# Optimization experiments

Measured on AMD Instinct MI355X. Metric: run time of the kernel, lower is better.

## Reference

```python
import jax, jax.numpy as jnp
import numpy as np

NUM_HEADS = 16
NUM_HIDDENS = 1024
NEG_INF = -1e6


def setup_inputs() -> dict:
    key = jax.random.key(0)
    ks = jax.random.split(key, 8)
    B, S, D = 2, 2048, NUM_HIDDENS
    scale = 1.0 / np.sqrt(D)
    return {
        "q": jax.random.normal(ks[0], (B, S, D), jnp.float32),
        "k": jax.random.normal(ks[1], (B, S, D), jnp.float32),
        "v": jax.random.normal(ks[2], (B, S, D), jnp.float32),
        # nn.Linear weights have shape (out_features, in_features)
        "Wq": jax.random.normal(ks[3], (D, D), jnp.float32) * scale,
        "Wk": jax.random.normal(ks[4], (D, D), jnp.float32) * scale,
        "Wv": jax.random.normal(ks[5], (D, D), jnp.float32) * scale,
        "Wo": jax.random.normal(ks[6], (D, D), jnp.float32) * scale,
        "valid_len": jax.random.randint(ks[7], (B,), 1, 2048 + 1, jnp.int32),
    }


def _unpack_heads(x, nh):
    # (B, S, H) -> (B*nh, S, H//nh), matching Unpack_base_head
    B, S, H = x.shape
    return x.reshape(B, S, nh, H // nh).transpose(0, 2, 1, 3).reshape(B * nh, S, H // nh)


def _merge_heads(x, nh):
    # Faithful to Merge_base_head: (B*nh, S, dh) -> (B, nh, S, dh)
    # -> permute(0,2,3,1) -> (B, S, dh, nh) -> (B, S, dh*nh)
    Bnh, S, dh = x.shape
    B = Bnh // nh
    x = x.reshape(B, nh, S, dh).transpose(0, 2, 3, 1)
    return x.reshape(B, S, dh * nh)


def reference(q, k, v, Wq, Wk, Wv, Wo, valid_len):
    nh = NUM_HEADS
    # projections (bias=False); Linear: x @ W.T
    qh = _unpack_heads(q @ Wq.T, nh)  # (B*nh, S, dh)
    kh = _unpack_heads(k @ Wk.T, nh)
    vh = _unpack_heads(v @ Wv.T, nh)
    dh = qh.shape[-1]
    scores = jnp.einsum("bqd,bkd->bqk", qh, kh) / jnp.sqrt(jnp.float32(dh))
    # repeat_interleave valid_len by num_heads along dim 0
    vl = jnp.repeat(valid_len, nh)  # (B*nh,)
    key_pos = jnp.arange(scores.shape[-1])  # (S,)
    mask = key_pos[None, None, :] < vl[:, None, None]  # (B*nh, 1, S)
    scores = jnp.where(mask, scores, NEG_INF)
    attn = jax.nn.softmax(scores, axis=-1)  # dropout=0.0 (eval) -> identity
    out = jnp.einsum("bqk,bkd->bqd", attn, vh)  # (B*nh, S, dh)
    out = _merge_heads(out, nh) @ Wo.T  # (B, S, H)
    return out, attn
```

## Files before the change

kernel.cpp:

```cpp
#include <hip/hip_runtime.h>
#include <stdint.h>

#define SB 2048
#define DB 1024
#define NHB 16
#define DHB 64

typedef __attribute__((ext_vector_type(8))) short short8;
typedef __attribute__((ext_vector_type(4))) short short4v;
typedef __attribute__((ext_vector_type(4))) float f32x4;

#define SC2 0.18033688011112042f

__device__ __forceinline__ unsigned short f2bf(float f) {
  union { float f; uint32_t u; } v; v.f = f;
  uint32_t u = v.u;
  return (unsigned short)((u + 0x7FFFu + ((u >> 16) & 1u)) >> 16);
}

__device__ __forceinline__ void gld16(const void* g, void* l) {
  __builtin_amdgcn_global_load_lds(
      (const __attribute__((address_space(1))) void*)g,
      (__attribute__((address_space(3))) void*)l, 16, 0, 0);
}

__device__ __forceinline__ int xcd_swz(int bid, int nwg) {
  return (bid & 7) * (nwg >> 3) + (bid >> 3);
}

struct ConvArgs {
  const float* s[6];
  unsigned short* d[6];
  int n[6];
};

__global__ __launch_bounds__(256) void conv_kernel(ConvArgs a,
                                                   const float* __restrict__ Wo,
                                                   unsigned short* __restrict__ Wob) {
  const int t = blockIdx.y;
  if (t == 6) {
    for (int i = blockIdx.x * 256 + threadIdx.x; i < DB * DB; i += gridDim.x * 256) {
      int o = i >> 10, cp = i & 1023;
      int src = (o << 10) + ((cp & 63) << 4) + (cp >> 6);
      Wob[i] = f2bf(Wo[src]);
    }
    return;
  }
  const float* __restrict__ src = a.s[t];
  unsigned short* __restrict__ dst = a.d[t];
  const int n8 = a.n[t] >> 3;
  for (int i = blockIdx.x * 256 + threadIdx.x; i < n8; i += gridDim.x * 256) {
    const f32x4* p = (const f32x4*)src + (size_t)i * 2;
    f32x4 x = p[0], y = p[1];
    short8 o;
    o[0] = (short)f2bf(x[0]); o[1] = (short)f2bf(x[1]);
    o[2] = (short)f2bf(x[2]); o[3] = (short)f2bf(x[3]);
    o[4] = (short)f2bf(y[0]); o[5] = (short)f2bf(y[1]);
    o[6] = (short)f2bf(y[2]); o[7] = (short)f2bf(y[3]);
    *(short8*)(dst + (size_t)i * 8) = o;
  }
}

struct GemmArgs {
  const unsigned short* A[3];
  const unsigned short* B[3];
  void* O[3];
  int mode[3];
};

__global__ __launch_bounds__(256) void gemm128(GemmArgs ga) {
  __shared__ unsigned short SH[17408];
  unsigned short* Ab = SH;
  unsigned short* Bb = SH + 8192;

  const int z = blockIdx.y;
  const unsigned short* __restrict__ A = ga.A[z];
  const unsigned short* __restrict__ Bw = ga.B[z];
  const int mode = ga.mode[z];

  const int tid = threadIdx.x;
  const int w = tid >> 6, lane = tid & 63;
  const int g = lane >> 4, li = lane & 15;
  const int wm = w >> 1, wn = w & 1;
  const int l = xcd_swz(blockIdx.x, 256);
  const int m0 = (l >> 3) * 128, n0 = (l & 7) * 128;

  const int srow = lane >> 3;
  const int sg = (lane & 7) ^ srow;

  f32x4 acc[4][4];
  #pragma unroll
  for (int i = 0; i < 4; ++i)
    #pragma unroll
    for (int j = 0; j < 4; ++j)
      #pragma unroll
      for (int e = 0; e < 4; ++e) acc[i][j][e] = 0.f;

  for (int k0 = 0; k0 < DB; k0 += 64) {
    __syncthreads();
    #pragma unroll
    for (int i = 0; i < 4; ++i) {
      int c = w * 4 + i;
      gld16(A + (size_t)(m0 + c * 8 + srow) * DB + k0 + sg * 8, Ab + c * 512);
      gld16(Bw + (size_t)(n0 + c * 8 + srow) * DB + k0 + sg * 8, Bb + c * 512);
    }
    __syncthreads();
    short8 af[4][2], bf[4][2];
    #pragma unroll
    for (int mf = 0; mf < 4; ++mf)
      #pragma unroll
      for (int ks = 0; ks < 2; ++ks)
        af[mf][ks] = *(const short8*)&Ab[(wm * 64 + mf * 16 + li) * 64 +
                                         (((ks * 4 + g) ^ (li & 7)) << 3)];
    #pragma unroll
    for (int nf = 0; nf < 4; ++nf)
      #pragma unroll
      for (int ks = 0; ks < 2; ++ks)
        bf[nf][ks] = *(const short8*)&Bb[(wn * 64 + nf * 16 + li) * 64 +
                                         (((ks * 4 + g) ^ (li & 7)) << 3)];
    __builtin_amdgcn_s_setprio(1);
    #pragma unroll
    for (int ks = 0; ks < 2; ++ks)
      #pragma unroll
      for (int mf = 0; mf < 4; ++mf)
        #pragma unroll
        for (int nf = 0; nf < 4; ++nf)
          acc[mf][nf] = __builtin_amdgcn_mfma_f32_16x16x32_bf16(
              af[mf][ks], bf[nf][ks], acc[mf][nf], 0, 0, 0);
    __builtin_amdgcn_s_setprio(0);
  }

  if (mode == 0) {
    unsigned short* O = (unsigned short*)ga.O[z];
    #pragma unroll
    for (int mf = 0; mf < 4; ++mf)
      #pragma unroll
      for (int nf = 0; nf < 4; ++nf)
        #pragma unroll
        for (int r = 0; r < 4; ++r) {
          int row = m0 + wm * 64 + mf * 16 + g * 4 + r;
          int col = n0 + wn * 64 + nf * 16 + li;
          int b_ = row >> 11, s_ = row & 2047;
          int h = col >> 6, dp = col & 63;
          O[((size_t)(b_ * NHB + h) * SB + s_) * DHB + dp] = f2bf(acc[mf][nf][r]);
        }
  } else {
    unsigned short* O = (unsigned short*)ga.O[z];
    __syncthreads();
    #pragma unroll
    for (int mf = 0; mf < 4; ++mf)
      #pragma unroll
      for (int nf = 0; nf < 4; ++nf) {
        short4v pk;
        #pragma unroll
        for (int r = 0; r < 4; ++r) pk[r] = (short)f2bf(acc[mf][nf][r]);
        *(short4v*)&SH[(size_t)(wn * 64 + nf * 16 + li) * 136 +
                       wm * 64 + mf * 16 + g * 4] = pk;
      }
    __syncthreads();
    int c = tid >> 1, rh = tid & 1;
    int col = n0 + c;
    int h = col >> 6, dp = col & 63;
    int b_ = m0 >> 11, s0 = (m0 & 2047) + rh * 64;
    unsigned short* dst = O + ((size_t)(b_ * NHB + h) * DHB + dp) * SB + s0;
    #pragma unroll
    for (int j = 0; j < 8; ++j)
      *(short8*)(dst + j * 8) = *(const short8*)&SH[c * 136 + rh * 64 + j * 8];
  }
}

__global__ __launch_bounds__(256) void attn_kernel(
    const unsigned short* __restrict__ Qh, const unsigned short* __restrict__ Kh,
    const unsigned short* __restrict__ Vt, const int* __restrict__ valid_len,
    float* __restrict__ attn_out, unsigned short* __restrict__ Mg)
{
  __shared__ unsigned short Kb[2][4096];
  __shared__ unsigned short Vb[2][4096];
  __shared__ unsigned short P[128][72];

  const int tid = threadIdx.x;
  const int wave = tid >> 6, lane = tid & 63;
  const int g = lane >> 4, li = lane & 15;
  const int lsw = xcd_swz(blockIdx.x, 512);
  const int xcd = lsw >> 6, j = lsw & 63;
  const int bh = ((j >> 5) << 4) + xcd * 2 + ((j >> 4) & 1);
  const int q0 = (j & 15) * 128;
  const int b_ = bh >> 4;
  const int vl = valid_len[b_];
  const int nkt = min(32, (vl + 63) >> 6);

  const int srow = lane >> 3;
  const int sg = (lane & 7) ^ srow;

  const size_t kbase = (size_t)bh * SB * DHB;
  const size_t vbase = (size_t)bh * DHB * SB;

  short8 qa[2][2];
  #pragma unroll
  for (int qf = 0; qf < 2; ++qf)
    #pragma unroll
    for (int ks = 0; ks < 2; ++ks)
      qa[qf][ks] = *(const short8*)(
          Qh + ((size_t)bh * SB + q0 + wave * 32 + qf * 16 + li) * DHB +
          ks * 32 + g * 8);

  float lQ[2] = {0.f, 0.f};

  {
    const int c = wave * 2;
    gld16(Kh + kbase + (size_t)(c * 8 + srow) * DHB + sg * 8, &Kb[0][c * 512]);
    gld16(Kh + kbase + (size_t)((c + 1) * 8 + srow) * DHB + sg * 8,
          &Kb[0][(c + 1) * 512]);
    int cur = 0;
    for (int kti = 0; kti < nkt; ++kti) {
      __syncthreads();
      if (kti + 1 < nkt) {
        int kn = (kti + 1) * 64;
        gld16(Kh + kbase + (size_t)(kn + c * 8 + srow) * DHB + sg * 8,
              &Kb[cur ^ 1][c * 512]);
        gld16(Kh + kbase + (size_t)(kn + (c + 1) * 8 + srow) * DHB + sg * 8,
              &Kb[cur ^ 1][(c + 1) * 512]);
      }
      const int kt = kti * 64;
      f32x4 sc[2][4];
      #pragma unroll
      for (int qf = 0; qf < 2; ++qf)
        #pragma unroll
        for (int nf = 0; nf < 4; ++nf)
          #pragma unroll
          for (int e = 0; e < 4; ++e) sc[qf][nf][e] = 0.f;
      __builtin_amdgcn_s_setprio(1);
      #pragma unroll
      for (int ks = 0; ks < 2; ++ks)
        #pragma unroll
        for (int nf = 0; nf < 4; ++nf) {
          short8 kbf = *(const short8*)&Kb[cur][(nf * 16 + li) * 64 +
                                               (((ks * 4 + g) ^ (li & 7)) << 3)];
          #pragma unroll
          for (int qf = 0; qf < 2; ++qf)
            sc[qf][nf] = __builtin_amdgcn_mfma_f32_16x16x32_bf16(
                kbf, qa[qf][ks], sc[qf][nf], 0, 0, 0);
        }
      __builtin_amdgcn_s_setprio(0);
      if (kt + 64 <= vl) {
        #pragma unroll
        for (int qf = 0; qf < 2; ++qf) {
          float la = 0.f;
          #pragma unroll
          for (int nf = 0; nf < 4; ++nf)
            #pragma unroll
            for (int r = 0; r < 4; ++r) la += exp2f(sc[qf][nf][r] * SC2);
          lQ[qf] += la;
        }
      } else {
        #pragma unroll
        for (int qf = 0; qf < 2; ++qf) {
          float la = 0.f;
          #pragma unroll
          for (int nf = 0; nf < 4; ++nf)
            #pragma unroll
            for (int r = 0; r < 4; ++r) {
              int key = kt + nf * 16 + g * 4 + r;
              float s2 = (key < vl) ? sc[qf][nf][r] * SC2 : -1.5e6f;
              la += exp2f(s2);
            }
          lQ[qf] += la;
        }
      }
      cur ^= 1;
    }
  }
  __syncthreads();

  float rlQ[2];
  #pragma unroll
  for (int qf = 0; qf < 2; ++qf) {
    float L = lQ[qf];
    L += __shfl_xor(L, 16);
    L += __shfl_xor(L, 32);
    rlQ[qf] = 1.f / L;
  }

  f32x4 oacc[2][4];
  #pragma unroll
  for (int qf = 0; qf < 2; ++qf)
    #pragma unroll
    for (int nf = 0; nf < 4; ++nf)
      #pragma unroll
      for (int e = 0; e < 4; ++e) oacc[qf][nf][e] = 0.f;

  {
    const int c = wave * 2;
    gld16(Kh + kbase + (size_t)(c * 8 + srow) * DHB + sg * 8, &Kb[0][c * 512]);
    gld16(Kh + kbase + (size_t)((c + 1) * 8 + srow) * DHB + sg * 8,
          &Kb[0][(c + 1) * 512]);
    gld16(Vt + vbase + (size_t)(c * 8 + srow) * SB + sg * 8, &Vb[0][c * 512]);
    gld16(Vt + vbase + (size_t)((c + 1) * 8 + srow) * SB + sg * 8,
          &Vb[0][(c + 1) * 512]);
    asm volatile("s_waitcnt vmcnt(0)\n\ts_barrier" ::: "memory");
    int cur = 0;
    for (int kti = 0; kti < nkt; ++kti) {
      if (kti + 1 < nkt) {
        int kn = (kti + 1) * 64;
        gld16(Kh + kbase + (size_t)(kn + c * 8 + srow) * DHB + sg * 8,
              &Kb[cur ^ 1][c * 512]);
        gld16(Kh + kbase + (size_t)(kn + (c + 1) * 8 + srow) * DHB + sg * 8,
              &Kb[cur ^ 1][(c + 1) * 512]);
        gld16(Vt + vbase + (size_t)(c * 8 + srow) * SB + kn + sg * 8,
              &Vb[cur ^ 1][c * 512]);
        gld16(Vt + vbase + (size_t)((c + 1) * 8 + srow) * SB + kn + sg * 8,
              &Vb[cur ^ 1][(c + 1) * 512]);
      }
      const int kt = kti * 64;
      f32x4 sc[2][4];
      #pragma unroll
      for (int qf = 0; qf < 2; ++qf)
        #pragma unroll
        for (int nf = 0; nf < 4; ++nf)
          #pragma unroll
          for (int e = 0; e < 4; ++e) sc[qf][nf][e] = 0.f;
      __builtin_amdgcn_s_setprio(1);
      #pragma unroll
      for (int ks = 0; ks < 2; ++ks)
        #pragma unroll
        for (int nf = 0; nf < 4; ++nf) {
          short8 kbf = *(const short8*)&Kb[cur][(nf * 16 + li) * 64 +
                                               (((ks * 4 + g) ^ (li & 7)) << 3)];
          #pragma unroll
          for (int qf = 0; qf < 2; ++qf)
            sc[qf][nf] = __builtin_amdgcn_mfma_f32_16x16x32_bf16(
                kbf, qa[qf][ks], sc[qf][nf], 0, 0, 0);
        }
      __builtin_amdgcn_s_setprio(0);
      const bool fullt = (kt + 64 <= vl);
      #pragma unroll
      for (int qf = 0; qf < 2; ++qf) {
        const int qrow = q0 + wave * 32 + qf * 16 + li;
        #pragma unroll
        for (int nf = 0; nf < 4; ++nf) {
          short4v pk;
          if (fullt) {
            #pragma unroll
            for (int r = 0; r < 4; ++r) {
              float p = exp2f(sc[qf][nf][r] * SC2) * rlQ[qf];
              sc[qf][nf][r] = p;
              pk[r] = (short)f2bf(p);
            }
          } else {
            #pragma unroll
            for (int r = 0; r < 4; ++r) {
              int key = kt + nf * 16 + g * 4 + r;
              float s2 = (key < vl) ? sc[qf][nf][r] * SC2 : -1.5e6f;
              float p = exp2f(s2) * rlQ[qf];
              sc[qf][nf][r] = p;
              pk[r] = (short)f2bf(p);
            }
          }
          *(f32x4*)(attn_out + (size_t)bh * SB * SB + (size_t)qrow * SB +
                    kt + nf * 16 + g * 4) = sc[qf][nf];
          *(short4v*)&P[wave * 32 + qf * 16 + li][nf * 16 + g * 4] = pk;
        }
      }
      __builtin_amdgcn_s_setprio(1);
      #pragma unroll
      for (int ks = 0; ks < 2; ++ks) {
        short8 vbf[4];
        #pragma unroll
        for (int nf = 0; nf < 4; ++nf)
          vbf[nf] = *(const short8*)&Vb[cur][(nf * 16 + li) * 64 +
                                            (((ks * 4 + g) ^ (li & 7)) << 3)];
        #pragma unroll
        for (int qf = 0; qf < 2; ++qf) {
          short8 pa = *(const short8*)&P[wave * 32 + qf * 16 + li][ks * 32 + g * 8];
          #pragma unroll
          for (int nf = 0; nf < 4; ++nf)
            oacc[qf][nf] = __builtin_amdgcn_mfma_f32_16x16x32_bf16(
                pa, vbf[nf], oacc[qf][nf], 0, 0, 0);
        }
      }
      __builtin_amdgcn_s_setprio(0);
      asm volatile("s_waitcnt vmcnt(8)\n\ts_barrier" ::: "memory");
      cur ^= 1;
    }
  }

  {
    int c0 = nkt * 64;
    int rem4 = (SB - c0) >> 2;
    if (rem4 > 0) {
      f32x4 z;
      z[0] = 0.f; z[1] = 0.f; z[2] = 0.f; z[3] = 0.f;
      for (int row = 0; row < 128; ++row) {
        float* dst = attn_out + (size_t)bh * SB * SB + (size_t)(q0 + row) * SB + c0;
        for (int c = tid; c < rem4; c += 256)
          __builtin_nontemporal_store(z, (f32x4*)dst + c);
      }
    }
  }

  __syncthreads();
  const int h = bh & 15;
  #pragma unroll
  for (int qf = 0; qf < 2; ++qf)
    #pragma unroll
    for (int nf = 0; nf < 4; ++nf)
      #pragma unroll
      for (int r = 0; r < 4; ++r)
        P[wave * 32 + qf * 16 + g * 4 + r][nf * 16 + li] = f2bf(oacc[qf][nf][r]);
  __syncthreads();
  {
    int row = tid >> 1, half = (tid & 1) * 32;
    unsigned short* dst = Mg + ((size_t)b_ * SB + q0 + row) * DB + h * 64 + half;
    #pragma unroll
    for (int j2 = 0; j2 < 4; ++j2)
      *(short8*)(dst + j2 * 8) = *(const short8*)&P[row][half + j2 * 8];
  }
}

__global__ __launch_bounds__(256) void outproj_kernel(
    const unsigned short* __restrict__ A, const unsigned short* __restrict__ Bw,
    float* __restrict__ Out)
{
  __shared__ unsigned short SH[12288];
  unsigned short* Ab = SH;
  unsigned short* Bb = SH + 8192;

  const int tid = threadIdx.x;
  const int w = tid >> 6, lane = tid & 63;
  const int g = lane >> 4, li = lane & 15;
  const int wm = w >> 1, wn = w & 1;
  const int l = xcd_swz(blockIdx.x, 512);
  const int m0 = (l >> 4) * 128, n0 = (l & 15) * 64;

  const int srow = lane >> 3;
  const int sg = (lane & 7) ^ srow;

  int a_off[4][2], b_off[2][2];
  #pragma unroll
  for (int mf = 0; mf < 4; ++mf) {
    int row = wm * 64 + mf * 16 + li;
    #pragma unroll
    for (int ks = 0; ks < 2; ++ks)
      a_off[mf][ks] = row * 64 + (((ks * 4 + g) ^ (li & 7)) << 3);
  }
  #pragma unroll
  for (int nf = 0; nf < 2; ++nf) {
    int row = wn * 32 + nf * 16 + li;
    #pragma unroll
    for (int ks = 0; ks < 2; ++ks)
      b_off[nf][ks] = row * 64 + (((ks * 4 + g) ^ (li & 7)) << 3);
  }

  f32x4 acc[4][2];
  #pragma unroll
  for (int i = 0; i < 4; ++i)
    #pragma unroll
    for (int j = 0; j < 2; ++j)
      #pragma unroll
      for (int e = 0; e < 4; ++e) acc[i][j][e] = 0.f;

  for (int k0 = 0; k0 < DB; k0 += 64) {
    __syncthreads();
    #pragma unroll
    for (int i = 0; i < 4; ++i) {
      int c = w * 4 + i;
      gld16(A + (size_t)(m0 + c * 8 + srow) * DB + k0 + sg * 8, Ab + c * 512);
    }
    #pragma unroll
    for (int i = 0; i < 2; ++i) {
      int c = w * 2 + i;
      gld16(Bw + (size_t)(n0 + c * 8 + srow) * DB + k0 + sg * 8, Bb + c * 512);
    }
    __syncthreads();
    short8 af[4][2], bf[2][2];
    #pragma unroll
    for (int mf = 0; mf < 4; ++mf)
      #pragma unroll
      for (int ks = 0; ks < 2; ++ks)
        af[mf][ks] = *(const short8*)&Ab[a_off[mf][ks]];
    #pragma unroll
    for (int nf = 0; nf < 2; ++nf)
      #pragma unroll
      for (int ks = 0; ks < 2; ++ks)
        bf[nf][ks] = *(const short8*)&Bb[b_off[nf][ks]];
    __builtin_amdgcn_s_setprio(1);
    #pragma unroll
    for (int ks = 0; ks < 2; ++ks)
      #pragma unroll
      for (int mf = 0; mf < 4; ++mf)
        #pragma unroll
        for (int nf = 0; nf < 2; ++nf)
          acc[mf][nf] = __builtin_amdgcn_mfma_f32_16x16x32_bf16(
              af[mf][ks], bf[nf][ks], acc[mf][nf], 0, 0, 0);
    __builtin_amdgcn_s_setprio(0);
  }

  #pragma unroll
  for (int mf = 0; mf < 4; ++mf)
    #pragma unroll
    for (int nf = 0; nf < 2; ++nf)
      #pragma unroll
      for (int r = 0; r < 4; ++r) {
        int row = m0 + wm * 64 + mf * 16 + g * 4 + r;
        int col = n0 + wn * 32 + nf * 16 + li;
        Out[(size_t)row * DB + col] = acc[mf][nf][r];
      }
}

extern "C" void kernel_launch(void* const* d_in, const int* in_sizes, int n_in,
                              void* d_out, int out_size, void* d_ws, size_t ws_size,
                              hipStream_t stream) {
  const float* q  = (const float*)d_in[0];
  const float* k  = (const float*)d_in[1];
  const float* v  = (const float*)d_in[2];
  const float* Wq = (const float*)d_in[3];
  const float* Wk = (const float*)d_in[4];
  const float* Wv = (const float*)d_in[5];
  const float* Wo = (const float*)d_in[6];
  const int* vlen = (const int*)d_in[7];

  const size_t HS = (size_t)2 * NHB * SB * DHB;
  const size_t WS = (size_t)DB * DB;

  unsigned short* ws = (unsigned short*)d_ws;
  unsigned short* qb  = ws;
  unsigned short* kb  = qb + HS;
  unsigned short* vb  = kb + HS;
  unsigned short* Wqb = vb + HS;
  unsigned short* Wkb = Wqb + WS;
  unsigned short* Wvb = Wkb + WS;
  unsigned short* Wob = Wvb + WS;
  unsigned short* Qh  = Wob + WS;
  unsigned short* Kh  = Qh + HS;
  unsigned short* Vt  = Kh + HS;
  unsigned short* Mg  = qb;

  float* out  = (float*)d_out;
  float* attn = out + (size_t)2 * SB * DB;

  ConvArgs ca;
  ca.s[0] = q;  ca.d[0] = qb;  ca.n[0] = (int)HS;
  ca.s[1] = k;  ca.d[1] = kb;  ca.n[1] = (int)HS;
  ca.s[2] = v;  ca.d[2] = vb;  ca.n[2] = (int)HS;
  ca.s[3] = Wq; ca.d[3] = Wqb; ca.n[3] = (int)WS;
  ca.s[4] = Wk; ca.d[4] = Wkb; ca.n[4] = (int)WS;
  ca.s[5] = Wv; ca.d[5] = Wvb; ca.n[5] = (int)WS;

  GemmArgs pa;
  pa.A[0] = qb;  pa.A[1] = kb;  pa.A[2] = vb;
  pa.B[0] = Wqb; pa.B[1] = Wkb; pa.B[2] = Wvb;
  pa.O[0] = Qh;  pa.O[1] = Kh;  pa.O[2] = Vt;
  pa.mode[0] = 0; pa.mode[1] = 0; pa.mode[2] = 1;

  dim3 blk(256);
  conv_kernel<<<dim3(1024, 7), blk, 0, stream>>>(ca, Wo, Wob);
  gemm128<<<dim3(256, 3), blk, 0, stream>>>(pa);
  attn_kernel<<<dim3(512), blk, 0, stream>>>(Qh, Kh, Vt, vlen, attn, Mg);
  outproj_kernel<<<dim3(512), blk, 0, stream>>>(Mg, Wob, out);
}
```

Before: 221.3 us.

## Fuse fp32-to-bf16 conversion into projection GEMM tile loads

The separate conversion kernel is removed. The QKV projection GEMM now reads fp32 activations and weights directly, converts them with packed bf16 cvt instructions, and stores the result to LDS through registers instead of async global-to-LDS loads. The Wo conversion moves into an extra grid slice of the same launch. This drops one launch and the round trip of bf16 copies through global memory. In exchange, each tile reads twice the bytes per k-step, weights are reconverted by every block, and the loads are now synchronous.

```diff
diff --git a/kernel.cpp b/kernel.cpp
--- a/kernel.cpp
+++ b/kernel.cpp
@@ -18,6 +18,17 @@
   return (unsigned short)((u + 0x7FFFu + ((u >> 16) & 1u)) >> 16);
 }
 
+__device__ __forceinline__ short8 cvt8(const float* p) {
+  f32x4 a = *(const f32x4*)p;
+  f32x4 b = *(const f32x4*)(p + 4);
+  union { uint32_t u[4]; short8 s; } o;
+  asm("v_cvt_pk_bf16_f32 %0, %1, %2" : "=v"(o.u[0]) : "v"(a[0]), "v"(a[1]));
+  asm("v_cvt_pk_bf16_f32 %0, %1, %2" : "=v"(o.u[1]) : "v"(a[2]), "v"(a[3]));
+  asm("v_cvt_pk_bf16_f32 %0, %1, %2" : "=v"(o.u[2]) : "v"(b[0]), "v"(b[1]));
+  asm("v_cvt_pk_bf16_f32 %0, %1, %2" : "=v"(o.u[3]) : "v"(b[2]), "v"(b[3]));
+  return o.s;
+}
+
 __device__ __forceinline__ void gld16(const void* g, void* l) {
   __builtin_amdgcn_global_load_lds(
       (const __attribute__((address_space(1))) void*)g,
@@ -28,57 +39,37 @@
   return (bid & 7) * (nwg >> 3) + (bid >> 3);
 }
 
-struct ConvArgs {
-  const float* s[6];
-  unsigned short* d[6];
-  int n[6];
+struct PGArgs {
+  const float* A[3];
+  const float* B[3];
+  unsigned short* O[3];
+  int mode[3];
+  const float* Wo;
+  unsigned short* Wob;
 };
 
-__global__ __launch_bounds__(256) void conv_kernel(ConvArgs a,
-                                                   const float* __restrict__ Wo,
-                                                   unsigned short* __restrict__ Wob) {
-  const int t = blockIdx.y;
-  if (t == 6) {
-    for (int i = blockIdx.x * 256 + threadIdx.x; i < DB * DB; i += gridDim.x * 256) {
+__global__ __launch_bounds__(256) void projfused(PGArgs ga) {
+  __shared__ unsigned short SH[17408];
+
+  const int z = blockIdx.y;
+  const int tid = threadIdx.x;
+
+  if (z == 3) {
+    for (int i = blockIdx.x * 256 + tid; i < DB * DB; i += 256 * 256) {
       int o = i >> 10, cp = i & 1023;
       int src = (o << 10) + ((cp & 63) << 4) + (cp >> 6);
-      Wob[i] = f2bf(Wo[src]);
+      ga.Wob[i] = f2bf(ga.Wo[src]);
     }
     return;
   }
-  const float* __restrict__ src = a.s[t];
-  unsigned short* __restrict__ dst = a.d[t];
-  const int n8 = a.n[t] >> 3;
-  for (int i = blockIdx.x * 256 + threadIdx.x; i < n8; i += gridDim.x * 256) {
-    const f32x4* p = (const f32x4*)src + (size_t)i * 2;
-    f32x4 x = p[0], y = p[1];
-    short8 o;
-    o[0] = (short)f2bf(x[0]); o[1] = (short)f2bf(x[1]);
-    o[2] = (short)f2bf(x[2]); o[3] = (short)f2bf(x[3]);
-    o[4] = (short)f2bf(y[0]); o[5] = (short)f2bf(y[1]);
-    o[6] = (short)f2bf(y[2]); o[7] = (short)f2bf(y[3]);
-    *(short8*)(dst + (size_t)i * 8) = o;
-  }
-}
-
-struct GemmArgs {
-  const unsigned short* A[3];
-  const unsigned short* B[3];
-  void* O[3];
-  int mode[3];
-};
-
-__global__ __launch_bounds__(256) void gemm128(GemmArgs ga) {
-  __shared__ unsigned short SH[17408];
+
   unsigned short* Ab = SH;
   unsigned short* Bb = SH + 8192;
 
-  const int z = blockIdx.y;
-  const unsigned short* __restrict__ A = ga.A[z];
-  const unsigned short* __restrict__ Bw = ga.B[z];
+  const float* __restrict__ Af = ga.A[z];
+  const float* __restrict__ Bf = ga.B[z];
   const int mode = ga.mode[z];
 
-  const int tid = threadIdx.x;
   const int w = tid >> 6, lane = tid & 63;
   const int g = lane >> 4, li = lane & 15;
   const int wm = w >> 1, wn = w & 1;
@@ -101,8 +92,10 @@
     #pragma unroll
     for (int i = 0; i < 4; ++i) {
       int c = w * 4 + i;
-      gld16(A + (size_t)(m0 + c * 8 + srow) * DB + k0 + sg * 8, Ab + c * 512);
-      gld16(Bw + (size_t)(n0 + c * 8 + srow) * DB + k0 + sg * 8, Bb + c * 512);
+      short8 va = cvt8(Af + (size_t)(m0 + c * 8 + srow) * DB + k0 + sg * 8);
+      short8 vb = cvt8(Bf + (size_t)(n0 + c * 8 + srow) * DB + k0 + sg * 8);
+      *(short8*)&Ab[c * 512 + lane * 8] = va;
+      *(short8*)&Bb[c * 512 + lane * 8] = vb;
     }
     __syncthreads();
     short8 af[4][2], bf[4][2];
@@ -131,7 +124,7 @@
   }
 
   if (mode == 0) {
-    unsigned short* O = (unsigned short*)ga.O[z];
+    unsigned short* O = ga.O[z];
     #pragma unroll
     for (int mf = 0; mf < 4; ++mf)
       #pragma unroll
@@ -145,7 +138,7 @@
           O[((size_t)(b_ * NHB + h) * SB + s_) * DHB + dp] = f2bf(acc[mf][nf][r]);
         }
   } else {
-    unsigned short* O = (unsigned short*)ga.O[z];
+    unsigned short* O = ga.O[z];
     __syncthreads();
     #pragma unroll
     for (int mf = 0; mf < 4; ++mf)
@@ -523,38 +516,24 @@
   const size_t WS = (size_t)DB * DB;
 
   unsigned short* ws = (unsigned short*)d_ws;
-  unsigned short* qb  = ws;
-  unsigned short* kb  = qb + HS;
-  unsigned short* vb  = kb + HS;
-  unsigned short* Wqb = vb + HS;
-  unsigned short* Wkb = Wqb + WS;
-  unsigned short* Wvb = Wkb + WS;
-  unsigned short* Wob = Wvb + WS;
+  unsigned short* Wob = ws;
   unsigned short* Qh  = Wob + WS;
   unsigned short* Kh  = Qh + HS;
   unsigned short* Vt  = Kh + HS;
-  unsigned short* Mg  = qb;
+  unsigned short* Mg  = Vt + HS;
 
   float* out  = (float*)d_out;
   float* attn = out + (size_t)2 * SB * DB;
 
-  ConvArgs ca;
-  ca.s[0] = q;  ca.d[0] = qb;  ca.n[0] = (int)HS;
-  ca.s[1] = k;  ca.d[1] = kb;  ca.n[1] = (int)HS;
-  ca.s[2] = v;  ca.d[2] = vb;  ca.n[2] = (int)HS;
-  ca.s[3] = Wq; ca.d[3] = Wqb; ca.n[3] = (int)WS;
-  ca.s[4] = Wk; ca.d[4] = Wkb; ca.n[4] = (int)WS;
-  ca.s[5] = Wv; ca.d[5] = Wvb; ca.n[5] = (int)WS;
-
-  GemmArgs pa;
-  pa.A[0] = qb;  pa.A[1] = kb;  pa.A[2] = vb;
-  pa.B[0] = Wqb; pa.B[1] = Wkb; pa.B[2] = Wvb;
-  pa.O[0] = Qh;  pa.O[1] = Kh;  pa.O[2] = Vt;
+  PGArgs pa;
+  pa.A[0] = q;  pa.A[1] = k;  pa.A[2] = v;
+  pa.B[0] = Wq; pa.B[1] = Wk; pa.B[2] = Wv;
+  pa.O[0] = Qh; pa.O[1] = Kh; pa.O[2] = Vt;
   pa.mode[0] = 0; pa.mode[1] = 0; pa.mode[2] = 1;
+  pa.Wo = Wo; pa.Wob = Wob;
 
   dim3 blk(256);
-  conv_kernel<<<dim3(1024, 7), blk, 0, stream>>>(ca, Wo, Wob);
-  gemm128<<<dim3(256, 3), blk, 0, stream>>>(pa);
+  projfused<<<dim3(256, 4), blk, 0, stream>>>(pa);
   attn_kernel<<<dim3(512), blk, 0, stream>>>(Qh, Kh, Vt, vlen, attn, Mg);
   outproj_kernel<<<dim3(512), blk, 0, stream>>>(Mg, Wob, out);
 }
```

After: 236.3 us. 6.8% more time.
